# Kernel tuning notes

Measured on AMD Instinct MI355X. Metric: run time of the kernel, lower is better.

The kernel has to match this reference:

```python
import jax, jax.numpy as jnp
import numpy as np

D_MODEL = 512
N_HEADS = 16
D_HEAD = D_MODEL // N_HEADS


def _relative_shift(pos_score):
    # pos_score: [B, H, T, T]  (Transformer-XL shift trick)
    B, H, T1, T2 = pos_score.shape
    padded = jnp.pad(pos_score, ((0, 0), (0, 0), (0, 0), (1, 0)))  # [B,H,T1,T2+1]
    padded = padded.reshape(B, H, T2 + 1, T1)
    return padded[:, :, 1:].reshape(B, H, T1, T2)


def setup_inputs() -> dict:
    key = jax.random.key(0)
    ks = jax.random.split(key, 12)
    B, T, D = 4, 1024, D_MODEL
    s = 1.0 / np.sqrt(D)
    return {
        "q": jax.random.normal(ks[0], (B, T, D), jnp.float32),
        "k": jax.random.normal(ks[1], (B, T, D), jnp.float32),
        "v": jax.random.normal(ks[2], (B, T, D), jnp.float32),
        "pos_embedding": jax.random.normal(ks[3], (B, T, D), jnp.float32),
        "Wq": jax.random.normal(ks[4], (D, D), jnp.float32) * s,
        "bq": jnp.zeros((D,), jnp.float32),
        "Wp": jax.random.normal(ks[5], (D, D), jnp.float32) * s,
        "Wf": jax.random.normal(ks[6], (D, D), jnp.float32) * s,
        "bf": jnp.zeros((D,), jnp.float32),
        "u_bias": jax.random.normal(ks[7], (N_HEADS, D_HEAD), jnp.float32) * s,
        "v_bias": jax.random.normal(ks[8], (N_HEADS, D_HEAD), jnp.float32) * s,
    }


def reference(q, k, v, pos_embedding, Wq, bq, Wp, Wf, bf, u_bias, v_bias):
    B, T, D = q.shape
    H, Dh = N_HEADS, D_HEAD
    sqrt_dim = jnp.asarray(np.sqrt(D_MODEL), q.dtype)
    # NOTE: original module uses linear_q for q, k AND v (faithful to source)
    qh = (q @ Wq + bq).reshape(B, T, H, Dh)            # [B,T,H,Dh]
    kh = (k @ Wq + bq).reshape(B, T, H, Dh)
    vh = (v @ Wq + bq).reshape(B, T, H, Dh)
    ph = (pos_embedding @ Wp).reshape(B, T, H, Dh)     # no bias

    content_score = jnp.einsum('bthd,bshd->bhts', qh + u_bias, kh)
    pos_score = jnp.einsum('bthd,bshd->bhts', qh + v_bias, ph)
    pos_score = _relative_shift(pos_score)

    score = (content_score + pos_score) / sqrt_dim     # [B,H,T,T]
    attn = jax.nn.softmax(score, axis=-1)              # dropout identity in eval
    context = jnp.einsum('bhts,bshd->bthd', attn, vh).reshape(B, T, D)
    return context @ Wf + bf
```

## Files before the change

### kernel.cpp

```cpp
#include <hip/hip_runtime.h>
#include <hip/hip_bf16.h>

typedef __bf16 bf16;
typedef bf16 bf16x8 __attribute__((ext_vector_type(8)));
typedef bf16 bf16x4 __attribute__((ext_vector_type(4)));
typedef float f32x4 __attribute__((ext_vector_type(4)));
typedef _Float16 f16x4 __attribute__((ext_vector_type(4)));

#define SCALE_LOG2 0.06376237f


__global__ __launch_bounds__(256) void prep_kernel(
    const float* __restrict__ Wq, const float* __restrict__ Wp, const float* __restrict__ Wf,
    bf16* __restrict__ WqT, bf16* __restrict__ WpT, bf16* __restrict__ WfT)
{
  const int tid = threadIdx.x;
  __shared__ bf16 t[64][72];
  const int m = blockIdx.x >> 6;
  const int tb = blockIdx.x & 63;
  const int tr = tb >> 3, tc = tb & 7;
  const float* W = (m == 0) ? Wq : (m == 1) ? Wp : Wf;
  bf16*        O = (m == 0) ? WqT : (m == 1) ? WpT : WfT;
  const int r = tid >> 2, cg = tid & 3;
  {
    const float* src = W + (size_t)(tr * 64 + r) * 512 + tc * 64 + cg * 16;
    f32x4 a = *(const f32x4*)src, b2 = *(const f32x4*)(src + 4);
    f32x4 c = *(const f32x4*)(src + 8), d = *(const f32x4*)(src + 12);
    bf16x8 lo, hi;
#pragma unroll
    for (int j = 0; j < 4; j++) { lo[j] = (bf16)a[j]; lo[4 + j] = (bf16)b2[j]; hi[j] = (bf16)c[j]; hi[4 + j] = (bf16)d[j]; }
    *(bf16x8*)(&t[r][cg * 16])     = lo;
    *(bf16x8*)(&t[r][cg * 16 + 8]) = hi;
  }
  __syncthreads();
  bf16x8 o0, o1;
#pragma unroll
  for (int j = 0; j < 8; j++) { o0[j] = t[cg * 16 + j][r]; o1[j] = t[cg * 16 + 8 + j][r]; }
  bf16* dst = O + (size_t)(tc * 64 + r) * 512 + tr * 64 + cg * 16;
  *(bf16x8*)dst = o0;
  *(bf16x8*)(dst + 8) = o1;
}

__global__ __launch_bounds__(256) void proj_gemm(
    const float* __restrict__ q, const float* __restrict__ k, const float* __restrict__ v,
    const float* __restrict__ pos,
    const bf16* __restrict__ WqT, const bf16* __restrict__ WpT, const float* __restrict__ bq,
    bf16* __restrict__ qh, bf16* __restrict__ kh, bf16* __restrict__ vT, bf16* __restrict__ phx)
{
  __shared__ bf16 As[128 * 72];
  __shared__ bf16 Bs[128 * 72];
  __shared__ bf16 vtile[128 * 132];
  const int tid = threadIdx.x;
  const int wave = tid >> 6, lane = tid & 63, quad = lane >> 4, ln = lane & 15;
  const int wg = blockIdx.x;
  const int xcd = wg & 7, sidx = wg >> 3;
  const int tn = sidx & 3;
  const int tm = xcd + ((sidx >> 2) << 3);
  const int kind = tm >> 5;
  const int rr0 = (tm & 31) * 128;
  const float* X = (kind == 0) ? q : (kind == 1) ? k : (kind == 2) ? v : pos;
  const bf16* WT = ((kind < 3) ? WqT : WpT) + (size_t)tn * 128 * 512;
  const int qn_ = (wave & 1) * 64;
  const int qr_ = (wave >> 1) * 64;
  const int srow = tid >> 2, scg = tid & 3;

  f32x4 acc[4][4] = {};

  f32x4  xa0[4], xa1[4];
  bf16x8 wr0[2], wr1[2];
  {
    const float* p0 = X + (size_t)(rr0 + srow) * 512 + scg * 16;
    const float* p1 = X + (size_t)(rr0 + srow + 64) * 512 + scg * 16;
#pragma unroll
    for (int u = 0; u < 4; u++) { xa0[u] = *(const f32x4*)(p0 + u * 4); xa1[u] = *(const f32x4*)(p1 + u * 4); }
    const bf16* w0 = WT + (size_t)srow * 512 + scg * 16;
    const bf16* w1 = WT + (size_t)(srow + 64) * 512 + scg * 16;
    wr0[0] = *(const bf16x8*)w0; wr0[1] = *(const bf16x8*)(w0 + 8);
    wr1[0] = *(const bf16x8*)w1; wr1[1] = *(const bf16x8*)(w1 + 8);
  }

  for (int kk = 0; kk < 8; kk++) {
    __syncthreads();
    {
      bf16x8 lo, hi;
#pragma unroll
      for (int j = 0; j < 4; j++) { lo[j] = (bf16)xa0[j >> 2 ? 0 : 0][0], lo[j] = (bf16)xa0[0][j]; }
#pragma unroll
      for (int j = 0; j < 4; j++) { lo[j] = (bf16)xa0[0][j]; lo[4 + j] = (bf16)xa0[1][j]; hi[j] = (bf16)xa0[2][j]; hi[4 + j] = (bf16)xa0[3][j]; }
      *(bf16x8*)(As + srow * 72 + scg * 16)     = lo;
      *(bf16x8*)(As + srow * 72 + scg * 16 + 8) = hi;
#pragma unroll
      for (int j = 0; j < 4; j++) { lo[j] = (bf16)xa1[0][j]; lo[4 + j] = (bf16)xa1[1][j]; hi[j] = (bf16)xa1[2][j]; hi[4 + j] = (bf16)xa1[3][j]; }
      *(bf16x8*)(As + (srow + 64) * 72 + scg * 16)     = lo;
      *(bf16x8*)(As + (srow + 64) * 72 + scg * 16 + 8) = hi;
      *(bf16x8*)(Bs + srow * 72 + scg * 16)            = wr0[0];
      *(bf16x8*)(Bs + srow * 72 + scg * 16 + 8)        = wr0[1];
      *(bf16x8*)(Bs + (srow + 64) * 72 + scg * 16)     = wr1[0];
      *(bf16x8*)(Bs + (srow + 64) * 72 + scg * 16 + 8) = wr1[1];
    }
    __syncthreads();

    if (kk < 7) {
      const int k0n = (kk + 1) * 64;
      const float* p0 = X + (size_t)(rr0 + srow) * 512 + k0n + scg * 16;
      const float* p1 = X + (size_t)(rr0 + srow + 64) * 512 + k0n + scg * 16;
#pragma unroll
      for (int u = 0; u < 4; u++) { xa0[u] = *(const f32x4*)(p0 + u * 4); xa1[u] = *(const f32x4*)(p1 + u * 4); }
      const bf16* w0 = WT + (size_t)srow * 512 + k0n + scg * 16;
      const bf16* w1 = WT + (size_t)(srow + 64) * 512 + k0n + scg * 16;
      wr0[0] = *(const bf16x8*)w0; wr0[1] = *(const bf16x8*)(w0 + 8);
      wr1[0] = *(const bf16x8*)w1; wr1[1] = *(const bf16x8*)(w1 + 8);
    }

#pragma unroll
    for (int ks = 0; ks < 2; ks++) {
      bf16x8 wf[4], xf[4];
#pragma unroll
      for (int i = 0; i < 4; i++) {
        wf[i] = *(const bf16x8*)(Bs + (qn_ + i * 16 + ln) * 72 + ks * 32 + quad * 8);
        xf[i] = *(const bf16x8*)(As + (qr_ + i * 16 + ln) * 72 + ks * 32 + quad * 8);
      }
#pragma unroll
      for (int i = 0; i < 4; i++)
#pragma unroll
        for (int j = 0; j < 4; j++)
          acc[i][j] = __builtin_amdgcn_mfma_f32_16x16x32_bf16(wf[i], xf[j], acc[i][j], 0, 0, 0);
    }
  }
  __syncthreads();

  if (kind == 2) {
#pragma unroll
    for (int i = 0; i < 4; i++) {
      const int nloc = qn_ + i * 16 + quad * 4;
      f32x4 b4 = *(const f32x4*)(bq + tn * 128 + nloc);
#pragma unroll
      for (int j = 0; j < 4; j++) {
        const int mloc = qr_ + j * 16 + ln;
        bf16x4 pk;
#pragma unroll
        for (int r = 0; r < 4; r++) pk[r] = (bf16)(acc[i][j][r] + b4[r]);
        *(bf16x4*)(vtile + mloc * 132 + nloc) = pk;
      }
    }
    __syncthreads();
    const int n = tid >> 1, mh = (tid & 1) * 64;
    const int bb2 = rr0 >> 10, tt0 = rr0 & 1023;
    bf16* vdst = vT + ((size_t)(bb2 * 16 + tn * 4 + (n >> 5)) * 32 + (n & 31)) * 1024 + tt0 + mh;
#pragma unroll
    for (int c = 0; c < 8; c++) {
      bf16x8 oc;
#pragma unroll
      for (int e = 0; e < 8; e++) oc[e] = vtile[(mh + c * 8 + e) * 132 + n];
      *(bf16x8*)(vdst + c * 8) = oc;
    }
  } else {
#pragma unroll
    for (int i = 0; i < 4; i++) {
      const int nn0 = tn * 128 + qn_ + i * 16 + quad * 4;
      const int dd0 = nn0 & 31, hh = nn0 >> 5;
      f32x4 b4 = {0.f, 0.f, 0.f, 0.f};
      if (kind < 3) b4 = *(const f32x4*)(bq + nn0);
#pragma unroll
      for (int j = 0; j < 4; j++) {
        const int rr = rr0 + qr_ + j * 16 + ln;
        const int bb = rr >> 10, tt = rr & 1023;
        const size_t base = (size_t)(bb * 16 + hh);
        bf16x4 pk;
#pragma unroll
        for (int r = 0; r < 4; r++) pk[r] = (bf16)(acc[i][j][r] + b4[r]);
        if (kind == 0)      *(bf16x4*)(qh + (base * 1024 + tt) * 32 + dd0) = pk;
        else if (kind == 1) *(bf16x4*)(kh + (base * 1024 + tt) * 32 + dd0) = pk;
        else {
          *(bf16x4*)(phx + (base * 2048 + tt) * 32 + dd0) = pk;
          if (tt <= 1021) *(bf16x4*)(phx + (base * 2048 + tt + 1025) * 32 + dd0) = pk;
          if (tt == 1023) {
            bf16x4 zz = {};
            *(bf16x4*)(phx + (base * 2048 + 1024) * 32 + dd0) = zz;
            *(bf16x4*)(phx + (base * 2048 + 2047) * 32 + dd0) = zz;
          }
        }
      }
    }
  }
}

__global__ __launch_bounds__(256, 4) void attn_kernel(
    const bf16* __restrict__ qh, const bf16* __restrict__ kh,
    const bf16* __restrict__ vT, const bf16* __restrict__ phx,
    const float* __restrict__ u_bias, const float* __restrict__ v_bias,
    float* __restrict__ Oa, float* __restrict__ Ob,
    float* __restrict__ la, float* __restrict__ lb)
{
  __shared__ bf16     kst[64 * 40];
  __shared__ bf16     phs[128 * 40];
  __shared__ bf16     vst[32 * 72];
  __shared__ _Float16 fs[4 * 16 * 84];
  __shared__ bf16     pb[4 * 16 * 72];

  const int tid = threadIdx.x;
  const int wave = tid >> 6, lane = tid & 63, quad = lane >> 4, ln = lane & 15;
  const int wg = blockIdx.x;
  const int bh = wg & 63;
  const int rest = wg >> 6;
  const int tq = rest & 15, sc = rest >> 4;
  const int h = bh & 15, b = bh >> 4;
  const int t0 = tq * 64;
  const bf16* qh_h  = qh  + (size_t)bh * 1024 * 32;
  const bf16* kh_h  = kh  + (size_t)bh * 1024 * 32;
  const bf16* vT_h  = vT  + (size_t)bh * 32 * 1024;
  const bf16* phx_h = phx + (size_t)bh * 2048 * 32;

  _Float16* fsw = fs + wave * 16 * 84;
  bf16*     pbw = pb + wave * 16 * 72;

  const int sr4 = tid >> 2, sc4 = tid & 3;
  const int sr8 = tid >> 3, sc8 = tid & 7;

  const int Ab  = quad * 4 + ((15 - ln) & ~3);
  const int msh = ((15 - ln) & 3) * 16;

  bf16x8 qu, qva, qvn;
  {
    const int t = t0 + wave * 16 + ln;
    bf16x8 q0 = *(const bf16x8*)(qh_h + (size_t)t * 32 + quad * 8);
    bf16x8 q1 = *(const bf16x8*)(qh_h + (size_t)(t + 1) * 32 + quad * 8);
    const float* ubp = u_bias + h * 32 + quad * 8;
    const float* vbp = v_bias + h * 32 + quad * 8;
#pragma unroll
    for (int j = 0; j < 8; j++) {
      qu[j]  = (bf16)(((float)q0[j] + ubp[j]) * SCALE_LOG2);
      qva[j] = (bf16)(((float)q0[j] + vbp[j]) * SCALE_LOG2);
      qvn[j] = (bf16)(((float)q1[j] + vbp[j]) * SCALE_LOG2);
    }
  }

  f32x4 O0 = {0.f, 0.f, 0.f, 0.f}, O1 = {0.f, 0.f, 0.f, 0.f};
  float l_lane = 0.0f;
  const f32x4 zf = {0.f, 0.f, 0.f, 0.f};

  const int si0 = sc * 8;

  bf16x8 g0, g1, g2, g3;
  {
    const int s0p = si0 * 64, jbp = s0p - t0 + 960;
    g0 = *(const bf16x8*)(kh_h  + (size_t)(s0p + sr4) * 32 + sc4 * 8);
    g1 = *(const bf16x8*)(phx_h + (size_t)(jbp + sr4) * 32 + sc4 * 8);
    g2 = *(const bf16x8*)(phx_h + (size_t)(jbp + 64 + sr4) * 32 + sc4 * 8);
    g3 = *(const bf16x8*)(vT_h  + (size_t)sr8 * 1024 + s0p + sc8 * 8);
  }

  for (int si = si0; si < si0 + 8; si++) {
    const int s0 = si * 64;
    const int jbase = s0 - t0 + 960;
    const int jb0 = jbase + (3 - wave) * 16;

    __syncthreads();

    *(bf16x8*)(kst + sr4 * 40 + sc4 * 8)        = g0;
    *(bf16x8*)(phs + sr4 * 40 + sc4 * 8)        = g1;
    *(bf16x8*)(phs + (64 + sr4) * 40 + sc4 * 8) = g2;
    *(bf16x8*)(vst + sr8 * 72 + sc8 * 8)        = g3;

    __syncthreads();

    if (si != si0 + 7) {
      const int s0n = s0 + 64, jbn = jbase + 64;
      g0 = *(const bf16x8*)(kh_h  + (size_t)(s0n + sr4) * 32 + sc4 * 8);
      g1 = *(const bf16x8*)(phx_h + (size_t)(jbn + sr4) * 32 + sc4 * 8);
      g2 = *(const bf16x8*)(phx_h + (size_t)(jbn + 64 + sr4) * 32 + sc4 * 8);
      g3 = *(const bf16x8*)(vT_h  + (size_t)sr8 * 1024 + s0n + sc8 * 8);
    }

#pragma unroll
    for (int i = 0; i < 5; i++) {
      const int row = (3 - wave + i) * 16 + ln;
      bf16x8 pbf = *(const bf16x8*)(phs + row * 40 + quad * 8);
      bf16x8 bsel = (jb0 + i * 16 >= 1024) ? qvn : qva;
      f32x4 f = __builtin_amdgcn_mfma_f32_16x16x32_bf16(pbf, bsel, zf, 0, 0, 0);
      f16x4 fh;
#pragma unroll
      for (int r = 0; r < 4; r++) fh[r] = (_Float16)f[r];
      *(f16x4*)(fsw + ln * 84 + i * 16 + quad * 4) = fh;
    }

    f32x4 c[4];
#pragma unroll
    for (int cs = 0; cs < 4; cs++) {
      bf16x8 kbf = *(const bf16x8*)(kst + (cs * 16 + ln) * 40 + quad * 8);
      c[cs] = __builtin_amdgcn_mfma_f32_16x16x32_bf16(kbf, qu, zf, 0, 0, 0);
    }

    const _Float16* rowp = fsw + ln * 84;
#pragma unroll
    for (int cs = 0; cs < 4; cs++) {
      const uint64_t v0 = *(const uint64_t*)(rowp + cs * 16 + Ab);
      const uint64_t v1 = *(const uint64_t*)(rowp + cs * 16 + Ab + 4);
      union { uint64_t u; f16x4 v; } W;
      W.u = (v0 >> msh) | ((v1 << 1) << (63 - msh));
      bf16x4 pk;
#pragma unroll
      for (int r = 0; r < 4; r++) {
        const float p = __builtin_amdgcn_exp2f(c[cs][r] + (float)W.v[r]);
        l_lane += p;
        pk[r] = (bf16)p;
      }
      *(bf16x4*)(pbw + ln * 72 + cs * 16 + quad * 4) = pk;
    }

#pragma unroll
    for (int kb = 0; kb < 2; kb++) {
      bf16x8 a  = *(const bf16x8*)(pbw + ln * 72 + kb * 32 + quad * 8);
      bf16x8 b0 = *(const bf16x8*)(vst + ln * 72 + kb * 32 + quad * 8);
      bf16x8 b1 = *(const bf16x8*)(vst + (16 + ln) * 72 + kb * 32 + quad * 8);
      O0 = __builtin_amdgcn_mfma_f32_16x16x32_bf16(a, b0, O0, 0, 0, 0);
      O1 = __builtin_amdgcn_mfma_f32_16x16x32_bf16(a, b1, O1, 0, 0, 0);
    }
  }

  l_lane += __shfl_xor(l_lane, 16);
  l_lane += __shfl_xor(l_lane, 32);

  float* Op = sc ? Ob : Oa;
  float* lp = sc ? lb : la;
#pragma unroll
  for (int r = 0; r < 4; r++) {
    const int t = t0 + wave * 16 + quad * 4 + r;
    const size_t o = ((size_t)(b * 1024 + t)) * 512 + h * 32;
    Op[o + ln]      = O0[r];
    Op[o + 16 + ln] = O1[r];
  }
  if (lane < 16) lp[(size_t)bh * 1024 + t0 + wave * 16 + lane] = l_lane;
}

__global__ __launch_bounds__(256) void out_gemm(
    const float* __restrict__ Oa, const float* __restrict__ Ob,
    const float* __restrict__ la, const float* __restrict__ lb,
    const bf16* __restrict__ WfT, const float* __restrict__ bfv,
    float* __restrict__ out)
{
  __shared__ bf16 As[64 * 40];
  __shared__ bf16 Bs[128 * 40];
  __shared__ float linv[16 * 64];
  const int tid = threadIdx.x;
  const int wave = tid >> 6, lane = tid & 63, quad = lane >> 4, ln = lane & 15;
  const int wg = blockIdx.x;
  const int xcd = wg & 7, sidx = wg >> 3;
  const int tn = sidx & 3;
  const int tm = xcd + ((sidx >> 2) << 3);
  const int rr0 = tm * 64;
  const bf16* WT = WfT + (size_t)tn * 128 * 512;
  const int qm = (wave & 1) * 32, qn = (wave >> 1) * 64;
  const int srow = tid >> 2, scg = tid & 3;

  f32x4 a0, a1, c0, c1;
  bf16x8 b0r, b1r;
  {
    const float* pa  = Oa + (size_t)(rr0 + srow) * 512 + scg * 8;
    const float* pcb = Ob + (size_t)(rr0 + srow) * 512 + scg * 8;
    a0 = *(const f32x4*)pa;  a1 = *(const f32x4*)(pa + 4);
    c0 = *(const f32x4*)pcb; c1 = *(const f32x4*)(pcb + 4);
    b0r = *(const bf16x8*)(WT + (size_t)srow * 512 + scg * 8);
    b1r = *(const bf16x8*)(WT + (size_t)(srow + 64) * 512 + scg * 8);
  }

  for (int e = tid; e < 1024; e += 256) {
    const int hh = e >> 6, r = e & 63;
    const int row = rr0 + r;
    const int b_ = row >> 10, t_ = row & 1023;
    const size_t li = ((size_t)(b_ * 16 + hh)) * 1024 + t_;
    linv[e] = 1.0f / (la[li] + lb[li]);
  }

  f32x4 acc[2][4] = {};
  for (int kk = 0; kk < 16; kk++) {
    __syncthreads();
    {
      const float s = linv[kk * 64 + srow];
      bf16x8 t8;
#pragma unroll
      for (int j = 0; j < 4; j++) {
        t8[j]     = (bf16)((a0[j] + c0[j]) * s);
        t8[4 + j] = (bf16)((a1[j] + c1[j]) * s);
      }
      *(bf16x8*)(As + srow * 40 + scg * 8)        = t8;
      *(bf16x8*)(Bs + srow * 40 + scg * 8)        = b0r;
      *(bf16x8*)(Bs + (srow + 64) * 40 + scg * 8) = b1r;
    }
    __syncthreads();

    if (kk < 15) {
      const int k0n = (kk + 1) * 32;
      const float* pa  = Oa + (size_t)(rr0 + srow) * 512 + k0n + scg * 8;
      const float* pcb = Ob + (size_t)(rr0 + srow) * 512 + k0n + scg * 8;
      a0 = *(const f32x4*)pa;  a1 = *(const f32x4*)(pa + 4);
      c0 = *(const f32x4*)pcb; c1 = *(const f32x4*)(pcb + 4);
      b0r = *(const bf16x8*)(WT + (size_t)srow * 512 + k0n + scg * 8);
      b1r = *(const bf16x8*)(WT + (size_t)(srow + 64) * 512 + k0n + scg * 8);
    }

    bf16x8 af[2], bfm[4];
#pragma unroll
    for (int i = 0; i < 2; i++)
      af[i] = *(const bf16x8*)(As + (qm + i * 16 + ln) * 40 + quad * 8);
#pragma unroll
    for (int j = 0; j < 4; j++)
      bfm[j] = *(const bf16x8*)(Bs + (qn + j * 16 + ln) * 40 + quad * 8);
#pragma unroll
    for (int i = 0; i < 2; i++)
#pragma unroll
      for (int j = 0; j < 4; j++)
        acc[i][j] = __builtin_amdgcn_mfma_f32_16x16x32_bf16(af[i], bfm[j], acc[i][j], 0, 0, 0);
  }

#pragma unroll
  for (int i = 0; i < 2; i++)
#pragma unroll
    for (int j = 0; j < 4; j++) {
      const int nn = tn * 128 + qn + j * 16 + ln;
      const float bias = bfv[nn];
#pragma unroll
      for (int r = 0; r < 4; r++) {
        const int rr = rr0 + qm + i * 16 + quad * 4 + r;
        out[(size_t)rr * 512 + nn] = acc[i][j][r] + bias;
      }
    }
}

extern "C" void kernel_launch(void* const* d_in, const int* in_sizes, int n_in,
                              void* d_out, int out_size, void* d_ws, size_t ws_size,
                              hipStream_t stream) {
  const float* q   = (const float*)d_in[0];
  const float* k   = (const float*)d_in[1];
  const float* v   = (const float*)d_in[2];
  const float* pe  = (const float*)d_in[3];
  const float* Wq  = (const float*)d_in[4];
  const float* bq  = (const float*)d_in[5];
  const float* Wp  = (const float*)d_in[6];
  const float* Wf  = (const float*)d_in[7];
  const float* bfv = (const float*)d_in[8];
  const float* ub  = (const float*)d_in[9];
  const float* vb  = (const float*)d_in[10];

  bf16* ws  = (bf16*)d_ws;
  bf16* qh  = ws;
  bf16* kh  = qh + 2097152;
  bf16* vT  = kh + 2097152;
  bf16* phx = vT + 2097152;
  bf16* WqT = phx + 4194304;
  bf16* WpT = WqT + 262144;
  bf16* WfT = WpT + 262144;
  float* Oa = (float*)(WfT + 262144);
  float* Ob = Oa + 2097152;
  float* la = Ob + 2097152;
  float* lb = la + 65536;

  prep_kernel<<<192, 256, 0, stream>>>(Wq, Wp, Wf, WqT, WpT, WfT);
  proj_gemm<<<512, 256, 0, stream>>>(q, k, v, pe, WqT, WpT, bq, qh, kh, vT, phx);
  attn_kernel<<<2048, 256, 0, stream>>>(qh, kh, vT, phx, ub, vb, Oa, Ob, la, lb);
  out_gemm<<<256, 256, 0, stream>>>(Oa, Ob, la, lb, WfT, bfv, (float*)d_out);
}
```

Before: 162.0 us.

## Double-buffer attention LDS tiles, alias proj LDS, halve out_gemm tile rows

The attention loop now ping-pongs between two LDS buffers for K, positional and V tiles, which removes one barrier per iteration. proj_gemm aliases its transpose tile onto the A/B staging buffers to cut LDS footprint and raise occupancy. out_gemm switches to 32-row tiles with twice as many blocks to fill more CUs. Risks are more LDS use in attention, which could lower occupancy, and possible hazards from the aliased proj tile if the barriers are insufficient.

New measurement: 171.0 us. 5.5% more time.

```diff
diff --git a/kernel.cpp b/kernel.cpp
--- a/kernel.cpp
+++ b/kernel.cpp
@@ -47,9 +47,10 @@
     const bf16* __restrict__ WqT, const bf16* __restrict__ WpT, const float* __restrict__ bq,
     bf16* __restrict__ qh, bf16* __restrict__ kh, bf16* __restrict__ vT, bf16* __restrict__ phx)
 {
-  __shared__ bf16 As[128 * 72];
-  __shared__ bf16 Bs[128 * 72];
-  __shared__ bf16 vtile[128 * 132];
+  __shared__ bf16 ABs[2 * 128 * 72];
+  bf16* As = ABs;
+  bf16* Bs = ABs + 128 * 72;
+  bf16* vtile = ABs;
   const int tid = threadIdx.x;
   const int wave = tid >> 6, lane = tid & 63, quad = lane >> 4, ln = lane & 15;
   const int wg = blockIdx.x;
@@ -84,8 +85,6 @@
     {
       bf16x8 lo, hi;
 #pragma unroll
-      for (int j = 0; j < 4; j++) { lo[j] = (bf16)xa0[j >> 2 ? 0 : 0][0], lo[j] = (bf16)xa0[0][j]; }
-#pragma unroll
       for (int j = 0; j < 4; j++) { lo[j] = (bf16)xa0[0][j]; lo[4 + j] = (bf16)xa0[1][j]; hi[j] = (bf16)xa0[2][j]; hi[4 + j] = (bf16)xa0[3][j]; }
       *(bf16x8*)(As + srow * 72 + scg * 16)     = lo;
       *(bf16x8*)(As + srow * 72 + scg * 16 + 8) = hi;
@@ -192,9 +191,9 @@
     float* __restrict__ Oa, float* __restrict__ Ob,
     float* __restrict__ la, float* __restrict__ lb)
 {
-  __shared__ bf16     kst[64 * 40];
-  __shared__ bf16     phs[128 * 40];
-  __shared__ bf16     vst[32 * 72];
+  __shared__ bf16     kst[2][64 * 40];
+  __shared__ bf16     phs[2][128 * 40];
+  __shared__ bf16     vst[2][32 * 72];
   __shared__ _Float16 fs[4 * 16 * 84];
   __shared__ bf16     pb[4 * 16 * 72];
 
@@ -250,17 +249,20 @@
     g3 = *(const bf16x8*)(vT_h  + (size_t)sr8 * 1024 + s0p + sc8 * 8);
   }
 
+#pragma unroll 2
   for (int si = si0; si < si0 + 8; si++) {
+    const int buf = si & 1;
     const int s0 = si * 64;
     const int jbase = s0 - t0 + 960;
     const int jb0 = jbase + (3 - wave) * 16;
-
-    __syncthreads();
-
-    *(bf16x8*)(kst + sr4 * 40 + sc4 * 8)        = g0;
-    *(bf16x8*)(phs + sr4 * 40 + sc4 * 8)        = g1;
-    *(bf16x8*)(phs + (64 + sr4) * 40 + sc4 * 8) = g2;
-    *(bf16x8*)(vst + sr8 * 72 + sc8 * 8)        = g3;
+    bf16* kc = kst[buf];
+    bf16* pc = phs[buf];
+    bf16* vc = vst[buf];
+
+    *(bf16x8*)(kc + sr4 * 40 + sc4 * 8)        = g0;
+    *(bf16x8*)(pc + sr4 * 40 + sc4 * 8)        = g1;
+    *(bf16x8*)(pc + (64 + sr4) * 40 + sc4 * 8) = g2;
+    *(bf16x8*)(vc + sr8 * 72 + sc8 * 8)        = g3;
 
     __syncthreads();
 
@@ -275,7 +277,7 @@
 #pragma unroll
     for (int i = 0; i < 5; i++) {
       const int row = (3 - wave + i) * 16 + ln;
-      bf16x8 pbf = *(const bf16x8*)(phs + row * 40 + quad * 8);
+      bf16x8 pbf = *(const bf16x8*)(pc + row * 40 + quad * 8);
       bf16x8 bsel = (jb0 + i * 16 >= 1024) ? qvn : qva;
       f32x4 f = __builtin_amdgcn_mfma_f32_16x16x32_bf16(pbf, bsel, zf, 0, 0, 0);
       f16x4 fh;
@@ -287,7 +289,7 @@
     f32x4 c[4];
 #pragma unroll
     for (int cs = 0; cs < 4; cs++) {
-      bf16x8 kbf = *(const bf16x8*)(kst + (cs * 16 + ln) * 40 + quad * 8);
+      bf16x8 kbf = *(const bf16x8*)(kc + (cs * 16 + ln) * 40 + quad * 8);
       c[cs] = __builtin_amdgcn_mfma_f32_16x16x32_bf16(kbf, qu, zf, 0, 0, 0);
     }
 
@@ -311,8 +313,8 @@
 #pragma unroll
     for (int kb = 0; kb < 2; kb++) {
       bf16x8 a  = *(const bf16x8*)(pbw + ln * 72 + kb * 32 + quad * 8);
-      bf16x8 b0 = *(const bf16x8*)(vst + ln * 72 + kb * 32 + quad * 8);
-      bf16x8 b1 = *(const bf16x8*)(vst + (16 + ln) * 72 + kb * 32 + quad * 8);
+      bf16x8 b0 = *(const bf16x8*)(vc + ln * 72 + kb * 32 + quad * 8);
+      bf16x8 b1 = *(const bf16x8*)(vc + (16 + ln) * 72 + kb * 32 + quad * 8);
       O0 = __builtin_amdgcn_mfma_f32_16x16x32_bf16(a, b0, O0, 0, 0, 0);
       O1 = __builtin_amdgcn_mfma_f32_16x16x32_bf16(a, b1, O1, 0, 0, 0);
     }
@@ -339,51 +341,47 @@
     const bf16* __restrict__ WfT, const float* __restrict__ bfv,
     float* __restrict__ out)
 {
-  __shared__ bf16 As[64 * 40];
+  __shared__ bf16 As[32 * 40];
   __shared__ bf16 Bs[128 * 40];
-  __shared__ float linv[16 * 64];
+  __shared__ float linv[16 * 32];
   const int tid = threadIdx.x;
   const int wave = tid >> 6, lane = tid & 63, quad = lane >> 4, ln = lane & 15;
   const int wg = blockIdx.x;
   const int xcd = wg & 7, sidx = wg >> 3;
   const int tn = sidx & 3;
   const int tm = xcd + ((sidx >> 2) << 3);
-  const int rr0 = tm * 64;
+  const int rr0 = tm * 32;
   const bf16* WT = WfT + (size_t)tn * 128 * 512;
-  const int qm = (wave & 1) * 32, qn = (wave >> 1) * 64;
+  const int qm = (wave & 1) * 16, qn = (wave >> 1) * 64;
   const int srow = tid >> 2, scg = tid & 3;
-
-  f32x4 a0, a1, c0, c1;
+  const int srow8 = tid >> 3, scg8 = tid & 7;
+
+  f32x4 a0, c0;
   bf16x8 b0r, b1r;
   {
-    const float* pa  = Oa + (size_t)(rr0 + srow) * 512 + scg * 8;
-    const float* pcb = Ob + (size_t)(rr0 + srow) * 512 + scg * 8;
-    a0 = *(const f32x4*)pa;  a1 = *(const f32x4*)(pa + 4);
-    c0 = *(const f32x4*)pcb; c1 = *(const f32x4*)(pcb + 4);
+    a0 = *(const f32x4*)(Oa + (size_t)(rr0 + srow8) * 512 + scg8 * 4);
+    c0 = *(const f32x4*)(Ob + (size_t)(rr0 + srow8) * 512 + scg8 * 4);
     b0r = *(const bf16x8*)(WT + (size_t)srow * 512 + scg * 8);
     b1r = *(const bf16x8*)(WT + (size_t)(srow + 64) * 512 + scg * 8);
   }
 
-  for (int e = tid; e < 1024; e += 256) {
-    const int hh = e >> 6, r = e & 63;
+  for (int e = tid; e < 512; e += 256) {
+    const int hh = e >> 5, r = e & 31;
     const int row = rr0 + r;
     const int b_ = row >> 10, t_ = row & 1023;
     const size_t li = ((size_t)(b_ * 16 + hh)) * 1024 + t_;
     linv[e] = 1.0f / (la[li] + lb[li]);
   }
 
-  f32x4 acc[2][4] = {};
+  f32x4 acc[4] = {};
   for (int kk = 0; kk < 16; kk++) {
     __syncthreads();
     {
-      const float s = linv[kk * 64 + srow];
-      bf16x8 t8;
-#pragma unroll
-      for (int j = 0; j < 4; j++) {
-        t8[j]     = (bf16)((a0[j] + c0[j]) * s);
-        t8[4 + j] = (bf16)((a1[j] + c1[j]) * s);
-      }
-      *(bf16x8*)(As + srow * 40 + scg * 8)        = t8;
+      const float s = linv[kk * 32 + srow8];
+      bf16x4 t4;
+#pragma unroll
+      for (int j = 0; j < 4; j++) t4[j] = (bf16)((a0[j] + c0[j]) * s);
+      *(bf16x4*)(As + srow8 * 40 + scg8 * 4)      = t4;
       *(bf16x8*)(Bs + srow * 40 + scg * 8)        = b0r;
       *(bf16x8*)(Bs + (srow + 64) * 40 + scg * 8) = b1r;
     }
@@ -391,40 +389,32 @@
 
     if (kk < 15) {
       const int k0n = (kk + 1) * 32;
-      const float* pa  = Oa + (size_t)(rr0 + srow) * 512 + k0n + scg * 8;
-      const float* pcb = Ob + (size_t)(rr0 + srow) * 512 + k0n + scg * 8;
-      a0 = *(const f32x4*)pa;  a1 = *(const f32x4*)(pa + 4);
-      c0 = *(const f32x4*)pcb; c1 = *(const f32x4*)(pcb + 4);
+      a0 = *(const f32x4*)(Oa + (size_t)(rr0 + srow8) * 512 + k0n + scg8 * 4);
+      c0 = *(const f32x4*)(Ob + (size_t)(rr0 + srow8) * 512 + k0n + scg8 * 4);
       b0r = *(const bf16x8*)(WT + (size_t)srow * 512 + k0n + scg * 8);
       b1r = *(const bf16x8*)(WT + (size_t)(srow + 64) * 512 + k0n + scg * 8);
     }
 
-    bf16x8 af[2], bfm[4];
-#pragma unroll
-    for (int i = 0; i < 2; i++)
-      af[i] = *(const bf16x8*)(As + (qm + i * 16 + ln) * 40 + quad * 8);
+    bf16x8 af, bfm[4];
+    af = *(const bf16x8*)(As + (qm + ln) * 40 + quad * 8);
 #pragma unroll
     for (int j = 0; j < 4; j++)
       bfm[j] = *(const bf16x8*)(Bs + (qn + j * 16 + ln) * 40 + quad * 8);
 #pragma unroll
-    for (int i = 0; i < 2; i++)
-#pragma unroll
-      for (int j = 0; j < 4; j++)
-        acc[i][j] = __builtin_amdgcn_mfma_f32_16x16x32_bf16(af[i], bfm[j], acc[i][j], 0, 0, 0);
-  }
-
-#pragma unroll
-  for (int i = 0; i < 2; i++)
-#pragma unroll
-    for (int j = 0; j < 4; j++) {
-      const int nn = tn * 128 + qn + j * 16 + ln;
-      const float bias = bfv[nn];
-#pragma unroll
-      for (int r = 0; r < 4; r++) {
-        const int rr = rr0 + qm + i * 16 + quad * 4 + r;
-        out[(size_t)rr * 512 + nn] = acc[i][j][r] + bias;
-      }
-    }
+    for (int j = 0; j < 4; j++)
+      acc[j] = __builtin_amdgcn_mfma_f32_16x16x32_bf16(af, bfm[j], acc[j], 0, 0, 0);
+  }
+
+#pragma unroll
+  for (int j = 0; j < 4; j++) {
+    const int nn = tn * 128 + qn + j * 16 + ln;
+    const float bias = bfv[nn];
+#pragma unroll
+    for (int r = 0; r < 4; r++) {
+      const int rr = rr0 + qm + quad * 4 + r;
+      out[(size_t)rr * 512 + nn] = acc[j][r] + bias;
+    }
+  }
 }
 
 extern "C" void kernel_launch(void* const* d_in, const int* in_sizes, int n_in,
@@ -458,5 +448,5 @@
   prep_kernel<<<192, 256, 0, stream>>>(Wq, Wp, Wf, WqT, WpT, WfT);
   proj_gemm<<<512, 256, 0, stream>>>(q, k, v, pe, WqT, WpT, bq, qh, kh, vT, phx);
   attn_kernel<<<2048, 256, 0, stream>>>(qh, kh, vT, phx, ub, vb, Oa, Ob, la, lb);
-  out_gemm<<<256, 256, 0, stream>>>(Oa, Ob, la, lb, WfT, bfv, (float*)d_out);
+  out_gemm<<<512, 256, 0, stream>>>(Oa, Ob, la, lb, WfT, bfv, (float*)d_out);
 }
```
